# Kernel tuning notes

Measured on AMD Instinct MI355X. Metric: run time of the kernel, lower is better.

The kernel has to match this reference:

```python
import jax, jax.numpy as jnp
import numpy as np

N_SOURCE, N_TARGET, D, TFD, E = 100000, 50000, 128, 32, 640000


def setup_inputs() -> dict:
    key = jax.random.key(0)
    ks = jax.random.split(key, 6)
    x = jax.random.normal(ks[0], (N_SOURCE, D), dtype=jnp.float32)
    conv_weight = jax.random.normal(ks[1], (D, D), dtype=jnp.float32) / np.sqrt(D)
    conv_bias = jax.random.normal(ks[2], (D,), dtype=jnp.float32)
    target_feat = jax.random.normal(ks[3], (N_TARGET, TFD), dtype=jnp.float32)
    edge_weight = jax.random.uniform(ks[4], (E,), dtype=jnp.float32)
    inter_edge_index = jax.random.randint(ks[5], (2, E), 0, N_TARGET, dtype=jnp.int64)
    return {
        "x": x,
        "conv_weight": conv_weight,
        "conv_bias": conv_bias,
        "target_feat": target_feat,
        "edge_weight": edge_weight,
        "inter_edge_index": inter_edge_index,
    }


def reference(x, conv_weight, conv_bias, target_feat, edge_weight, inter_edge_index):
    n_source, _ = x.shape
    n_target = target_feat.shape[0]
    n_nodes = n_source + n_target  # padded graph: [source ; zero target rows]
    row = inter_edge_index[0]                 # source node ids
    col = inter_edge_index[1] + n_source      # shifted target node ids

    # GCN linear transform (zero-padded target rows stay zero, so only transform x)
    h = x @ conv_weight  # [n_source, D]

    # gcn_norm with remaining self-loops (fill value 1): deg = scatter_add over row + 1
    deg = jax.ops.segment_sum(edge_weight, row, num_segments=n_nodes) + 1.0
    dinv = jnp.where(deg > 0, jax.lax.rsqrt(deg), 0.0)
    norm = dinv[row] * edge_weight * dinv[col]  # [E]

    # message = norm * h[row]; aggregate (add) at targets. Self-loop messages on
    # targets are zero (zero-padded features), so they are omitted.
    msg = norm[:, None] * h[row]                       # [E, D]
    out_t = jax.ops.segment_sum(msg, col - n_source, num_segments=n_target)
    out_t = out_t + conv_bias

    out_t = jax.nn.relu(out_t)                         # if_relu=True
    return jnp.concatenate([out_t, jnp.abs(target_feat)], axis=1)  # mod='cat'
```

## Files before the change

### kernel.cpp

```cpp
#include <hip/hip_runtime.h>

#define N_SOURCE 100000
#define N_TARGET 50000
#define DIM 128
#define TFD 32
#define NE 640000
#define CAP 64

typedef __attribute__((ext_vector_type(8))) short short8;
typedef __attribute__((ext_vector_type(4))) float f32x4;

static constexpr size_t DEG_OFF   = 0;
static constexpr size_t CNT_OFF   = 262144;
static constexpr size_t XBF_OFF   = 524288;
static constexpr size_t WT_OFF    = 13324288;
static constexpr size_t PAIRS_OFF = 13357056;
static constexpr size_t ACC_OFF   = 38957056;

__device__ __forceinline__ unsigned short f2bf(float f) {
  unsigned u = __float_as_uint(f);
  return (unsigned short)((u + 0x7FFFu + ((u >> 16) & 1u)) >> 16);
}
__device__ __forceinline__ float bf2f(unsigned short u) {
  return __uint_as_float(((unsigned)u) << 16);
}

__global__ void prep(const float* __restrict__ x, const float* __restrict__ W,
                     unsigned short* __restrict__ xbf, unsigned short* __restrict__ wt) {
  int b = blockIdx.x, tid = threadIdx.x;
  if (b < 3125) {
    size_t t = (size_t)b * 256 + tid;
    const float4* x4 = (const float4*)x;
    float4 u = x4[2 * t], v = x4[2 * t + 1];
    ((ushort4*)xbf)[2 * t]     = make_ushort4(f2bf(u.x), f2bf(u.y), f2bf(u.z), f2bf(u.w));
    ((ushort4*)xbf)[2 * t + 1] = make_ushort4(f2bf(v.x), f2bf(v.y), f2bf(v.z), f2bf(v.w));
  } else {
    int t = (b - 3125) * 2048 + tid * 8;
    int n = t >> 7, k0 = t & 127;
#pragma unroll
    for (int j = 0; j < 8; ++j)
      wt[n * 128 + k0 + j] = f2bf(W[(k0 + j) * 128 + n]);
  }
}

__global__ void edges_pass(const int* __restrict__ row, const int* __restrict__ col,
                           const float* __restrict__ ew,
                           float* __restrict__ deg, int* __restrict__ cnt,
                           int2* __restrict__ pairs) {
  int e = blockIdx.x * blockDim.x + threadIdx.x;
  if (e >= NE) return;
  int r = row[e];
  int c = col[e];
  float w = ew[e];
  atomicAdd(&deg[r], w);
  int pos = atomicAdd(&cnt[c], 1);
  if (pos < CAP) pairs[(size_t)c * CAP + pos] = make_int2(r, __float_as_int(w));
}

__global__ __launch_bounds__(256) void gather_agg(const int* __restrict__ cnt,
                                                  const int2* __restrict__ pairs,
                                                  const float* __restrict__ deg,
                                                  const unsigned short* __restrict__ xbf,
                                                  unsigned short* __restrict__ accb) {
  int g = blockIdx.x * 8 + (threadIdx.x >> 5);
  int lane = threadIdx.x & 31;
  if (g >= N_TARGET) return;
  int n = cnt[g];
  if (n > CAP) n = CAP;
  const int2* __restrict__ pb = pairs + (size_t)g * CAP;
  float4 s = {0.f, 0.f, 0.f, 0.f};
  int e = 0;
  for (; e + 2 <= n; e += 2) {
    int4 q = *(const int4*)(pb + e);
    float nrm0 = rsqrtf(deg[q.x] + 1.0f) * __int_as_float(q.y);
    float nrm1 = rsqrtf(deg[q.z] + 1.0f) * __int_as_float(q.w);
    ushort4 a = *(const ushort4*)(xbf + (size_t)q.x * DIM + lane * 4);
    ushort4 b = *(const ushort4*)(xbf + (size_t)q.z * DIM + lane * 4);
    s.x = fmaf(nrm0, bf2f(a.x), s.x); s.y = fmaf(nrm0, bf2f(a.y), s.y);
    s.z = fmaf(nrm0, bf2f(a.z), s.z); s.w = fmaf(nrm0, bf2f(a.w), s.w);
    s.x = fmaf(nrm1, bf2f(b.x), s.x); s.y = fmaf(nrm1, bf2f(b.y), s.y);
    s.z = fmaf(nrm1, bf2f(b.z), s.z); s.w = fmaf(nrm1, bf2f(b.w), s.w);
  }
  if (e < n) {
    int2 p = pb[e];
    float nrm = rsqrtf(deg[p.x] + 1.0f) * __int_as_float(p.y);
    ushort4 a = *(const ushort4*)(xbf + (size_t)p.x * DIM + lane * 4);
    s.x = fmaf(nrm, bf2f(a.x), s.x); s.y = fmaf(nrm, bf2f(a.y), s.y);
    s.z = fmaf(nrm, bf2f(a.z), s.z); s.w = fmaf(nrm, bf2f(a.w), s.w);
  }
  *(ushort4*)(accb + (size_t)g * DIM + lane * 4) =
      make_ushort4(f2bf(s.x), f2bf(s.y), f2bf(s.z), f2bf(s.w));
}

__global__ __launch_bounds__(256) void gemm_mfma(
    const unsigned short* __restrict__ accb, const unsigned short* __restrict__ wt,
    const float* __restrict__ bias, const float* __restrict__ tf,
    float* __restrict__ out) {
  const int tid = threadIdx.x;
  const int wave = tid >> 6;
  const int lane = tid & 63;
  const int row0 = blockIdx.x * 64;

  {
    const float4* tf4 = (const float4*)tf;
    int base = blockIdx.x * 512 + tid * 2;
#pragma unroll
    for (int q = 0; q < 2; ++q) {
      int t = base + q;
      int i = t >> 3, j = t & 7;
      if (i < N_TARGET) {
        float4 v = tf4[t];
        v.x = fabsf(v.x); v.y = fabsf(v.y); v.z = fabsf(v.z); v.w = fabsf(v.w);
        ((float4*)(out + (size_t)i * (DIM + TFD) + DIM))[j] = v;
      }
    }
  }

  const int mrow = row0 + wave * 16 + (lane & 15);
  const int kg = lane >> 4;
  short8 a[4];
  {
    const unsigned short* ap = accb + (size_t)mrow * DIM + kg * 8;
#pragma unroll
    for (int t = 0; t < 4; ++t) a[t] = *(const short8*)(ap + t * 32);
  }

  const int ncol = lane & 15;
  const int orow0 = row0 + wave * 16 + (lane >> 4) * 4;
#pragma unroll
  for (int c = 0; c < 8; ++c) {
    int n = c * 16 + ncol;
    f32x4 acc = {0.f, 0.f, 0.f, 0.f};
    const unsigned short* bp = wt + (size_t)n * DIM + kg * 8;
#pragma unroll
    for (int t = 0; t < 4; ++t) {
      short8 b = *(const short8*)(bp + t * 32);
      acc = __builtin_amdgcn_mfma_f32_16x16x32_bf16(a[t], b, acc, 0, 0, 0);
    }
    float bv = bias[n];
#pragma unroll
    for (int r = 0; r < 4; ++r) {
      int i = orow0 + r;
      if (i < N_TARGET)
        out[(size_t)i * (DIM + TFD) + n] = fmaxf(acc[r] + bv, 0.f);
    }
  }
}

extern "C" void kernel_launch(void* const* d_in, const int* in_sizes, int n_in,
                              void* d_out, int out_size, void* d_ws, size_t ws_size,
                              hipStream_t stream) {
  const float* x    = (const float*)d_in[0];
  const float* W    = (const float*)d_in[1];
  const float* bias = (const float*)d_in[2];
  const float* tf   = (const float*)d_in[3];
  const float* ew   = (const float*)d_in[4];
  const int*   eidx = (const int*)d_in[5];
  const int* row = eidx;
  const int* col = eidx + NE;
  float* out = (float*)d_out;

  float*          deg   = (float*)((char*)d_ws + DEG_OFF);
  int*            cnt   = (int*)((char*)d_ws + CNT_OFF);
  unsigned short* xbf   = (unsigned short*)((char*)d_ws + XBF_OFF);
  unsigned short* wt    = (unsigned short*)((char*)d_ws + WT_OFF);
  int2*           pairs = (int2*)((char*)d_ws + PAIRS_OFF);
  unsigned short* accb  = (unsigned short*)((char*)d_ws + ACC_OFF);

  hipMemsetAsync(d_ws, 0, XBF_OFF, stream);

  prep<<<3133, 256, 0, stream>>>(x, W, xbf, wt);
  edges_pass<<<(NE + 255) / 256, 256, 0, stream>>>(row, col, ew, deg, cnt, pairs);
  gather_agg<<<(N_TARGET + 7) / 8, 256, 0, stream>>>(cnt, pairs, deg, xbf, accb);
  gemm_mfma<<<(N_TARGET + 63) / 64, 256, 0, stream>>>(accb, wt, bias, tf, out);
}
```

Before: 230.1 us.

## Fuse prep and edge pass, store edge ids in buckets, unroll gather by four

Merges the bf16 conversion kernel and the edge atomic pass into one launch, partitioning blocks by role, which removes a launch and lets the two independent phases overlap. Buckets now store 4-byte edge indices instead of 8-byte (row, weight) pairs, halving bucket write traffic and shrinking the workspace. The gather then does an extra indirection through row and edge_weight per edge. Its loop is unrolled to four edges per iteration to expose more memory-level parallelism.

```diff
diff --git a/kernel.cpp b/kernel.cpp
--- a/kernel.cpp
+++ b/kernel.cpp
@@ -15,7 +15,7 @@
 static constexpr size_t XBF_OFF   = 524288;
 static constexpr size_t WT_OFF    = 13324288;
 static constexpr size_t PAIRS_OFF = 13357056;
-static constexpr size_t ACC_OFF   = 38957056;
+static constexpr size_t ACC_OFF   = 26157056;
 
 __device__ __forceinline__ unsigned short f2bf(float f) {
   unsigned u = __float_as_uint(f);
@@ -25,41 +25,45 @@
   return __uint_as_float(((unsigned)u) << 16);
 }
 
-__global__ void prep(const float* __restrict__ x, const float* __restrict__ W,
-                     unsigned short* __restrict__ xbf, unsigned short* __restrict__ wt) {
+#define PREP_X_BLOCKS 3125
+#define PREP_W_BLOCKS 8
+#define EDGE_BLOCKS 2500
+#define TOTAL_BLOCKS (PREP_X_BLOCKS + PREP_W_BLOCKS + EDGE_BLOCKS)
+
+__global__ void prep_edges(const float* __restrict__ x, const float* __restrict__ W,
+                           const int* __restrict__ row, const int* __restrict__ col,
+                           const float* __restrict__ ew,
+                           unsigned short* __restrict__ xbf, unsigned short* __restrict__ wt,
+                           float* __restrict__ deg, int* __restrict__ cnt,
+                           int* __restrict__ pairs) {
   int b = blockIdx.x, tid = threadIdx.x;
-  if (b < 3125) {
+  if (b < PREP_X_BLOCKS) {
     size_t t = (size_t)b * 256 + tid;
     const float4* x4 = (const float4*)x;
     float4 u = x4[2 * t], v = x4[2 * t + 1];
     ((ushort4*)xbf)[2 * t]     = make_ushort4(f2bf(u.x), f2bf(u.y), f2bf(u.z), f2bf(u.w));
     ((ushort4*)xbf)[2 * t + 1] = make_ushort4(f2bf(v.x), f2bf(v.y), f2bf(v.z), f2bf(v.w));
-  } else {
-    int t = (b - 3125) * 2048 + tid * 8;
+  } else if (b < PREP_X_BLOCKS + PREP_W_BLOCKS) {
+    int t = (b - PREP_X_BLOCKS) * 2048 + tid * 8;
     int n = t >> 7, k0 = t & 127;
 #pragma unroll
     for (int j = 0; j < 8; ++j)
       wt[n * 128 + k0 + j] = f2bf(W[(k0 + j) * 128 + n]);
+  } else {
+    int e = (b - PREP_X_BLOCKS - PREP_W_BLOCKS) * 256 + tid;
+    if (e >= NE) return;
+    int c = col[e];
+    int pos = atomicAdd(&cnt[c], 1);
+    if (pos < CAP) pairs[(size_t)c * CAP + pos] = e;
+    atomicAdd(&deg[row[e]], ew[e]);
   }
 }
 
-__global__ void edges_pass(const int* __restrict__ row, const int* __restrict__ col,
-                           const float* __restrict__ ew,
-                           float* __restrict__ deg, int* __restrict__ cnt,
-                           int2* __restrict__ pairs) {
-  int e = blockIdx.x * blockDim.x + threadIdx.x;
-  if (e >= NE) return;
-  int r = row[e];
-  int c = col[e];
-  float w = ew[e];
-  atomicAdd(&deg[r], w);
-  int pos = atomicAdd(&cnt[c], 1);
-  if (pos < CAP) pairs[(size_t)c * CAP + pos] = make_int2(r, __float_as_int(w));
-}
-
 __global__ __launch_bounds__(256) void gather_agg(const int* __restrict__ cnt,
-                                                  const int2* __restrict__ pairs,
+                                                  const int* __restrict__ pairs,
                                                   const float* __restrict__ deg,
+                                                  const int* __restrict__ row,
+                                                  const float* __restrict__ ew,
                                                   const unsigned short* __restrict__ xbf,
                                                   unsigned short* __restrict__ accb) {
   int g = blockIdx.x * 8 + (threadIdx.x >> 5);
@@ -67,26 +71,36 @@
   if (g >= N_TARGET) return;
   int n = cnt[g];
   if (n > CAP) n = CAP;
-  const int2* __restrict__ pb = pairs + (size_t)g * CAP;
+  const int* __restrict__ pb = pairs + (size_t)g * CAP;
   float4 s = {0.f, 0.f, 0.f, 0.f};
   int e = 0;
-  for (; e + 2 <= n; e += 2) {
+  for (; e + 4 <= n; e += 4) {
     int4 q = *(const int4*)(pb + e);
-    float nrm0 = rsqrtf(deg[q.x] + 1.0f) * __int_as_float(q.y);
-    float nrm1 = rsqrtf(deg[q.z] + 1.0f) * __int_as_float(q.w);
-    ushort4 a = *(const ushort4*)(xbf + (size_t)q.x * DIM + lane * 4);
-    ushort4 b = *(const ushort4*)(xbf + (size_t)q.z * DIM + lane * 4);
-    s.x = fmaf(nrm0, bf2f(a.x), s.x); s.y = fmaf(nrm0, bf2f(a.y), s.y);
-    s.z = fmaf(nrm0, bf2f(a.z), s.z); s.w = fmaf(nrm0, bf2f(a.w), s.w);
-    s.x = fmaf(nrm1, bf2f(b.x), s.x); s.y = fmaf(nrm1, bf2f(b.y), s.y);
-    s.z = fmaf(nrm1, bf2f(b.z), s.z); s.w = fmaf(nrm1, bf2f(b.w), s.w);
+    int r0 = row[q.x], r1 = row[q.y], r2 = row[q.z], r3 = row[q.w];
+    float n0 = rsqrtf(deg[r0] + 1.0f) * ew[q.x];
+    float n1 = rsqrtf(deg[r1] + 1.0f) * ew[q.y];
+    float n2 = rsqrtf(deg[r2] + 1.0f) * ew[q.z];
+    float n3 = rsqrtf(deg[r3] + 1.0f) * ew[q.w];
+    ushort4 a0 = *(const ushort4*)(xbf + (size_t)r0 * DIM + lane * 4);
+    ushort4 a1 = *(const ushort4*)(xbf + (size_t)r1 * DIM + lane * 4);
+    ushort4 a2 = *(const ushort4*)(xbf + (size_t)r2 * DIM + lane * 4);
+    ushort4 a3 = *(const ushort4*)(xbf + (size_t)r3 * DIM + lane * 4);
+    s.x = fmaf(n0, bf2f(a0.x), s.x); s.y = fmaf(n0, bf2f(a0.y), s.y);
+    s.z = fmaf(n0, bf2f(a0.z), s.z); s.w = fmaf(n0, bf2f(a0.w), s.w);
+    s.x = fmaf(n1, bf2f(a1.x), s.x); s.y = fmaf(n1, bf2f(a1.y), s.y);
+    s.z = fmaf(n1, bf2f(a1.z), s.z); s.w = fmaf(n1, bf2f(a1.w), s.w);
+    s.x = fmaf(n2, bf2f(a2.x), s.x); s.y = fmaf(n2, bf2f(a2.y), s.y);
+    s.z = fmaf(n2, bf2f(a2.z), s.z); s.w = fmaf(n2, bf2f(a2.w), s.w);
+    s.x = fmaf(n3, bf2f(a3.x), s.x); s.y = fmaf(n3, bf2f(a3.y), s.y);
+    s.z = fmaf(n3, bf2f(a3.z), s.z); s.w = fmaf(n3, bf2f(a3.w), s.w);
   }
-  if (e < n) {
-    int2 p = pb[e];
-    float nrm = rsqrtf(deg[p.x] + 1.0f) * __int_as_float(p.y);
-    ushort4 a = *(const ushort4*)(xbf + (size_t)p.x * DIM + lane * 4);
-    s.x = fmaf(nrm, bf2f(a.x), s.x); s.y = fmaf(nrm, bf2f(a.y), s.y);
-    s.z = fmaf(nrm, bf2f(a.z), s.z); s.w = fmaf(nrm, bf2f(a.w), s.w);
+  for (; e < n; ++e) {
+    int pe = pb[e];
+    int r = row[pe];
+    float nr = rsqrtf(deg[r] + 1.0f) * ew[pe];
+    ushort4 a = *(const ushort4*)(xbf + (size_t)r * DIM + lane * 4);
+    s.x = fmaf(nr, bf2f(a.x), s.x); s.y = fmaf(nr, bf2f(a.y), s.y);
+    s.z = fmaf(nr, bf2f(a.z), s.z); s.w = fmaf(nr, bf2f(a.w), s.w);
   }
   *(ushort4*)(accb + (size_t)g * DIM + lane * 4) =
       make_ushort4(f2bf(s.x), f2bf(s.y), f2bf(s.z), f2bf(s.w));
@@ -164,13 +178,12 @@
   int*            cnt   = (int*)((char*)d_ws + CNT_OFF);
   unsigned short* xbf   = (unsigned short*)((char*)d_ws + XBF_OFF);
   unsigned short* wt    = (unsigned short*)((char*)d_ws + WT_OFF);
-  int2*           pairs = (int2*)((char*)d_ws + PAIRS_OFF);
+  int*            pairs = (int*)((char*)d_ws + PAIRS_OFF);
   unsigned short* accb  = (unsigned short*)((char*)d_ws + ACC_OFF);
 
   hipMemsetAsync(d_ws, 0, XBF_OFF, stream);
 
-  prep<<<3133, 256, 0, stream>>>(x, W, xbf, wt);
-  edges_pass<<<(NE + 255) / 256, 256, 0, stream>>>(row, col, ew, deg, cnt, pairs);
-  gather_agg<<<(N_TARGET + 7) / 8, 256, 0, stream>>>(cnt, pairs, deg, xbf, accb);
+  prep_edges<<<TOTAL_BLOCKS, 256, 0, stream>>>(x, W, row, col, ew, xbf, wt, deg, cnt, pairs);
+  gather_agg<<<(N_TARGET + 7) / 8, 256, 0, stream>>>(cnt, pairs, deg, row, ew, xbf, accb);
   gemm_mfma<<<(N_TARGET + 63) / 64, 256, 0, stream>>>(accb, wt, bias, tf, out);
 }
```

After: 235.5 us. 1.02x slower.
